# Performance work log

Measured on AMD Instinct MI355X. Metric: run time of the kernel, lower is better.

Reference implementation:

```python
import jax, jax.numpy as jnp
import numpy as np

H = 150
PASSES = 5
NSETS = 2
N = 50000
E = 400000
G = 64
SLOPE = 0.01  # torch leaky_relu default


def setup_inputs() -> dict:
    key = jax.random.key(0)
    ks = jax.random.split(key, 20)
    def u(k, shape, fan):
        lim = 1.0 / np.sqrt(fan)
        return jax.random.uniform(k, shape, jnp.float32, -lim, lim)
    return {
        "nodes": jax.random.normal(ks[0], (N, H), jnp.float32),
        "problem_type": jax.random.uniform(ks[1], (G, 1), jnp.float32),
        "edge_W": u(ks[2], (NSETS, H, H), H),
        "edge_b": u(ks[3], (NSETS, H), H),
        "gru_w_ih": u(ks[4], (3 * H, H), H),
        "gru_w_hh": u(ks[5], (3 * H, H), H),
        "gru_b_ih": u(ks[6], (3 * H,), H),
        "gru_b_hh": u(ks[7], (3 * H,), H),
        "fc1_w": u(ks[8], (80, 151), 151),
        "fc1_b": u(ks[9], (80,), 151),
        "fc2_w": u(ks[10], (80, 80), 80),
        "fc2_b": u(ks[11], (80,), 80),
        "fcL_w": u(ks[12], (10, 80), 80),
        "fcL_b": u(ks[13], (10,), 80),
        "edges": jax.random.randint(ks[14], (NSETS, E, 2), 0, N),
        "graph_ids": jnp.sort(jax.random.randint(ks[15], (N,), 0, G)),
        "tbptt": 0,
    }


def _gru_cell(x, h, w_ih, w_hh, b_ih, b_hh):
    gi = x @ w_ih.T + b_ih  # [N, 3H]
    gh = h @ w_hh.T + b_hh
    ir, iz, inn = jnp.split(gi, 3, axis=-1)
    hr, hz, hn = jnp.split(gh, 3, axis=-1)
    r = jax.nn.sigmoid(ir + hr)
    z = jax.nn.sigmoid(iz + hz)
    n = jnp.tanh(inn + r * hn)
    return (1.0 - z) * n + z * h


def reference(nodes, problem_type, edge_W, edge_b, gru_w_ih, gru_w_hh,
              gru_b_ih, gru_b_hh, fc1_w, fc1_b, fc2_w, fc2_b, fcL_w, fcL_b,
              edges, graph_ids, tbptt):
    n_sets = edge_W.shape[0]
    n_graphs = problem_type.shape[0]
    for j in range(PASSES):
        incoming = jnp.zeros_like(nodes)
        for k in range(n_sets):
            src = edges[k, :, 1]
            dst = edges[k, :, 0]
            # NOTE: in the source, the first Linear+leaky_relu result is
            # overwritten; the effective edge message is just the second Linear.
            y = nodes[src] @ edge_W[k].T + edge_b[k]  # [E, H]
            incoming = incoming.at[dst].add(y)
        nodes = _gru_cell(incoming, nodes, gru_w_ih, gru_w_hh, gru_b_ih, gru_b_hh)
        if tbptt == 1 and j < PASSES - 2:
            nodes = jax.lax.stop_gradient(nodes)
    g = jax.ops.segment_sum(nodes, graph_ids, num_segments=n_graphs)  # [G, H]
    g = jnp.log(g)
    g = jnp.where(jnp.isnan(g), 0.0, g)
    g = jax.nn.relu(g)
    x = jnp.concatenate([g, problem_type], axis=1)  # [G, 151]
    x = jax.nn.leaky_relu(x @ fc1_w.T + fc1_b, SLOPE)
    x = jax.nn.leaky_relu(x @ fc2_w.T + fc2_b, SLOPE)
    return x @ fcL_w.T + fcL_b  # [G, 10]
```

## Files before the change

### kernel.cpp

```cpp
#include <hip/hip_runtime.h>
#include <stdint.h>

#define NN 50000
#define H 150
#define NE 400000
#define NG 64
#define NPASS 5
#define KB 480
#define VC 640
#define NRB 391

typedef unsigned short u16;
typedef unsigned int u32;
typedef __attribute__((ext_vector_type(8))) short short8;
typedef __attribute__((ext_vector_type(4))) float float4v;
typedef __attribute__((ext_vector_type(4))) u32 uint4v;
typedef __attribute__((ext_vector_type(2))) u32 uint2v;

__device__ __forceinline__ u16 f2bf_rn(float x) {
  union { float f; u32 u; } v; v.f = x;
  u32 r = v.u + 0x7fffu + ((v.u >> 16) & 1u);
  return (u16)(r >> 16);
}
__device__ __forceinline__ float bf2f(u16 h) {
  union { u32 u; float f; } v; v.u = ((u32)h) << 16;
  return v.f;
}
__device__ __forceinline__ u32 packf(float v) {
  u16 hi = f2bf_rn(v);
  u16 lo = f2bf_rn(v - bf2f(hi));
  return (u32)hi | ((u32)lo << 16);
}
__device__ __forceinline__ float upk(u32 u) {
  union { u32 u; float f; } a, b;
  a.u = u << 16; b.u = u & 0xffff0000u;
  return a.f + b.f;
}
__device__ __forceinline__ void async16(const void* g, void* l) {
  __builtin_amdgcn_global_load_lds(
      (const __attribute__((address_space(1))) unsigned int*)(uintptr_t)g,
      (__attribute__((address_space(3))) unsigned int*)(uint32_t)(uintptr_t)l,
      16, 0, 0);
}

__global__ void hist_kernel(const int* __restrict__ edges, int* __restrict__ cnt) {
  int id = blockIdx.x * 256 + threadIdx.x;
  if (id >= 2 * NE) return;
  int dst = edges[id * 2];
  int set = id / NE;
  atomicAdd(&cnt[dst * 2 + set], 1);
}

__global__ __launch_bounds__(1024) void scan1_kernel(const int* __restrict__ cnt,
                                                     int* __restrict__ rowptr,
                                                     int* __restrict__ bsum, int n) {
  __shared__ int sd[1024];
  int t = threadIdx.x;
  int idx = blockIdx.x * 1024 + t;
  int v = (idx < n) ? cnt[idx] : 0;
  sd[t] = v;
  __syncthreads();
  for (int off = 1; off < 1024; off <<= 1) {
    int add = (t >= off) ? sd[t - off] : 0;
    __syncthreads();
    sd[t] += add;
    __syncthreads();
  }
  if (idx < n) rowptr[idx] = sd[t] - v;
  if (t == 1023) bsum[blockIdx.x] = sd[1023];
}

__global__ __launch_bounds__(128) void scan2_kernel(const int* __restrict__ bsum,
                                                    int* __restrict__ boff, int nb) {
  __shared__ int sd[128];
  int t = threadIdx.x;
  int v = (t < nb) ? bsum[t] : 0;
  sd[t] = v;
  __syncthreads();
  for (int off = 1; off < 128; off <<= 1) {
    int add = (t >= off) ? sd[t - off] : 0;
    __syncthreads();
    sd[t] += add;
    __syncthreads();
  }
  boff[t] = sd[t] - v;
}

__global__ void scan3_kernel(int* __restrict__ rowptr, const int* __restrict__ boff, int n) {
  int idx = blockIdx.x * 256 + threadIdx.x;
  if (idx < n) rowptr[idx] += boff[idx >> 10];
}

__global__ void total_kernel(int* __restrict__ rowptr, const int* __restrict__ boff, int n, int nb) {
  if (threadIdx.x == 0 && blockIdx.x == 0) rowptr[n] = boff[nb];
}

__global__ void copy_int_kernel(const int* __restrict__ a, int* __restrict__ b, int n) {
  int id = blockIdx.x * 256 + threadIdx.x;
  if (id < n) b[id] = a[id];
}

__global__ void fill_kernel(const int* __restrict__ edges, int* __restrict__ cursor,
                            u16* __restrict__ colbuf) {
  int id = blockIdx.x * 256 + threadIdx.x;
  if (id >= 2 * NE) return;
  int dst = edges[id * 2];
  int src = edges[id * 2 + 1];
  int set = id / NE;
  int pos = atomicAdd(&cursor[dst * 2 + set], 1);
  colbuf[pos] = (u16)src;
}

__global__ void bounds_kernel(const int* __restrict__ gids, int* __restrict__ gstart) {
  int g = threadIdx.x;
  if (g > NG) return;
  int lo = 0, hi = NN;
  while (lo < hi) { int m = (lo + hi) >> 1; if (gids[m] < g) lo = m + 1; else hi = m; }
  gstart[g] = lo;
}

__global__ void build_B_kernel(const float* __restrict__ wih, const float* __restrict__ whh,
                               const float* __restrict__ eW,
                               u16* __restrict__ Bh, u16* __restrict__ Bl) {
  int id = blockIdx.x * 256 + threadIdx.x;
  if (id >= VC * KB) return;
  int v = id / KB, k = id % KB;
  int g = (v >> 4) & 3, c = (v >> 6) * 16 + (v & 15);
  int seg = k / 160, kk = k % 160;
  float val = 0.f;
  if (c < H && kk < H) {
    if (seg < 2) {
      if (g < 3) {
        const float* wr = wih + (size_t)(g * H + c) * H;
        const float* wc = eW + (size_t)seg * H * H + kk;
        float acc = 0.f;
        for (int t = 0; t < H; t++) acc += wr[t] * wc[(size_t)t * H];
        val = acc;
      }
    } else {
      if (g == 0) val = whh[(size_t)c * H + kk];
      else if (g == 1) val = whh[(size_t)(H + c) * H + kk];
      else if (g == 3) val = whh[(size_t)(2 * H + c) * H + kk];
    }
  }
  u16 h = f2bf_rn(val);
  Bh[id] = h;
  Bl[id] = f2bf_rn(val - bf2f(h));
}

__global__ void build_coef_kernel(const float* __restrict__ wih,
                                  const float* __restrict__ eb,
                                  const float* __restrict__ bih, const float* __restrict__ bhh,
                                  float* __restrict__ coefs) {
  int id = threadIdx.x + blockIdx.x * 256;
  if (id >= VC) return;
  int g = id / 160, c = id % 160;
  float u0 = 0.f, u1 = 0.f, bs = 0.f;
  if (c < H) {
    if (g < 3) {
      const float* wr = wih + (size_t)(g * H + c) * H;
      for (int t = 0; t < H; t++) { u0 += wr[t] * eb[t]; u1 += wr[t] * eb[H + t]; }
    }
    if (g == 0) bs = bih[c] + bhh[c];
    else if (g == 1) bs = bih[H + c] + bhh[H + c];
    else if (g == 2) bs = bih[2 * H + c];
    else bs = bhh[2 * H + c];
  }
  coefs[id] = u0;
  coefs[VC + id] = u1;
  coefs[2 * VC + id] = bs;
}

__global__ void init_nodes_kernel(const float* __restrict__ nin,
                                  u32* __restrict__ npkA, u32* __restrict__ npkB) {
  int id = blockIdx.x * 256 + threadIdx.x;
  if (id >= NN * 160) return;
  int r = id / 160, c = id % 160;
  if (c < H) {
    npkA[id] = packf(nin[(size_t)r * H + c]);
  } else {
    npkA[id] = 0;
    npkB[id] = 0;
  }
}

__global__ void pad_S_kernel(u32* __restrict__ Snp) {
  int id = blockIdx.x * 256 + threadIdx.x;
  if (id >= NN * 20) return;
  int r = id / 20, rem = id % 20;
  int set = rem / 10, t = rem % 10;
  Snp[(size_t)r * 320 + set * 160 + H + t] = 0;
}

__global__ __launch_bounds__(256) void gather_kernel(
    const u32* __restrict__ npk, const int* __restrict__ rowptr,
    const u16* __restrict__ colbuf, u32* __restrict__ Snp) {
  int gtid = blockIdx.x * 256 + threadIdx.x;
  int wid = gtid >> 6;
  if (wid >= 2 * NN) return;
  int node = wid >> 1, set = wid & 1;
  int lane = gtid & 63;
  int s = rowptr[2 * node + set], e = rowptr[2 * node + set + 1];
  int deg = e - s;
  int cA = 2 * lane, cC = 128 + lane;
  bool okC = (cC < H);
  float aA = 0.f, aB = 0.f, aC = 0.f;
  for (int base = 0; base < deg; base += 64) {
    int rem = min(64, deg - base);
    u32 srcv = 0;
    if (lane < rem) srcv = (u32)colbuf[s + base + lane];
    int i = 0;
    for (; i + 3 < rem; i += 4) {
      u32 r0 = (u32)__builtin_amdgcn_readlane((int)srcv, i);
      u32 r1 = (u32)__builtin_amdgcn_readlane((int)srcv, i + 1);
      u32 r2 = (u32)__builtin_amdgcn_readlane((int)srcv, i + 2);
      u32 r3 = (u32)__builtin_amdgcn_readlane((int)srcv, i + 3);
      const u32* p0 = npk + (size_t)r0 * 160;
      const u32* p1 = npk + (size_t)r1 * 160;
      const u32* p2 = npk + (size_t)r2 * 160;
      const u32* p3 = npk + (size_t)r3 * 160;
      uint2v v0 = *(const uint2v*)(p0 + cA);
      uint2v v1 = *(const uint2v*)(p1 + cA);
      uint2v v2 = *(const uint2v*)(p2 + cA);
      uint2v v3 = *(const uint2v*)(p3 + cA);
      u32 w0 = 0, w1 = 0, w2 = 0, w3 = 0;
      if (okC) { w0 = p0[cC]; w1 = p1[cC]; w2 = p2[cC]; w3 = p3[cC]; }
      aA += upk(v0.x) + upk(v1.x);
      aB += upk(v0.y) + upk(v1.y);
      if (okC) aC += upk(w0) + upk(w1);
      aA += upk(v2.x) + upk(v3.x);
      aB += upk(v2.y) + upk(v3.y);
      if (okC) aC += upk(w2) + upk(w3);
    }
    for (; i + 1 < rem; i += 2) {
      u32 r0 = (u32)__builtin_amdgcn_readlane((int)srcv, i);
      u32 r1 = (u32)__builtin_amdgcn_readlane((int)srcv, i + 1);
      const u32* p0 = npk + (size_t)r0 * 160;
      const u32* p1 = npk + (size_t)r1 * 160;
      uint2v v0 = *(const uint2v*)(p0 + cA);
      uint2v v1 = *(const uint2v*)(p1 + cA);
      aA += upk(v0.x) + upk(v1.x);
      aB += upk(v0.y) + upk(v1.y);
      if (okC) aC += upk(p0[cC]) + upk(p1[cC]);
    }
    if (i < rem) {
      u32 r0 = (u32)__builtin_amdgcn_readlane((int)srcv, i);
      const u32* p0 = npk + (size_t)r0 * 160;
      uint2v v0 = *(const uint2v*)(p0 + cA);
      aA += upk(v0.x);
      aB += upk(v0.y);
      if (okC) aC += upk(p0[cC]);
    }
  }
  u32* o = Snp + (size_t)node * 320 + set * 160;
  o[cA] = packf(aA);
  o[cA + 1] = packf(aB);
  if (okC) o[cC] = packf(aC);
}


template<int KT>
__device__ __forceinline__ void stage_fn(
    const u32* __restrict__ Snp, const u32* __restrict__ npkc,
    const u16* __restrict__ Bhp, const u16* __restrict__ Blp,
    char* Ab, char* Bb, int tid, int w, int r0, int ccb) {
  #pragma unroll
  for (int i = 0; i < 4; i++) {
    int cl = i * 256 + tid;
    int row = cl >> 3;
    int q = (cl & 7) ^ (row & 7);
    int rg = min(r0 + row, NN - 1);
    if constexpr (KT < 10)
      async16(Snp + (size_t)rg * 320 + KT * 32 + q * 4, Ab + i * 4096 + w * 1024);
    else
      async16(npkc + (size_t)rg * 160 + (KT - 10) * 32 + q * 4, Ab + i * 4096 + w * 1024);
  }
  constexpr int koffB = (KT < 10) ? KT * 32 : 320 + (KT - 10) * 32;
  constexpr int skipg = (KT < 10) ? 3 : 2;
  #pragma unroll
  for (int i = 0; i < 2; i++) {
    int cl = i * 256 + tid;
    int row = cl >> 2;
    int q = (cl & 3) ^ ((row >> 1) & 3);
    if (((row >> 4) & 3) != skipg) {
      size_t gb = (size_t)(ccb * 128 + row) * KB + koffB + q * 8;
      int lb = i * 4096 + w * 1024;
      async16(Bhp + gb, Bb + lb);
      async16(Blp + gb, Bb + 8192 + lb);
    }
  }
}

template<int KTn>
__device__ __forceinline__ void read_frags_fn(
    const char* Ab, const char* Bb, int m, int quad, int mrow0, int nco0,
    uint4v (&A0)[4], uint4v (&A1)[4], short8 (&RBh)[3], short8 (&RBl)[3]) {
  #pragma unroll
  for (int jj = 0; jj < 3; jj++) {
    const int jsel = (jj == 2) ? ((KTn < 10) ? 2 : 3) : jj;
    int br = nco0 + jsel * 16 + m;
    int bd = br * 64 + ((quad ^ ((br >> 1) & 3)) * 16);
    RBh[jj] = *(const short8*)(Bb + bd);
    RBl[jj] = *(const short8*)(Bb + 8192 + bd);
  }
  #pragma unroll
  for (int mt = 0; mt < 4; mt++) {
    int r = mrow0 + mt * 16 + m;
    A0[mt] = *(const uint4v*)(Ab + r * 128 + (((2 * quad) ^ (r & 7)) * 16));
    A1[mt] = *(const uint4v*)(Ab + r * 128 + (((2 * quad + 1) ^ (r & 7)) * 16));
  }
}

template<int KT>
__device__ __forceinline__ void mfma_fn(
    const uint4v (&A0)[4], const uint4v (&A1)[4],
    const short8 (&MBh)[3], const short8 (&MBl)[3], float4v (&acc)[4][4]) {
  #pragma unroll
  for (int mt = 0; mt < 4; mt++) {
    u32 uu[8] = {A0[mt].x, A0[mt].y, A0[mt].z, A0[mt].w,
                 A1[mt].x, A1[mt].y, A1[mt].z, A1[mt].w};
    short8 ah, al;
    #pragma unroll
    for (int e2 = 0; e2 < 8; e2++) {
      ah[e2] = (short)(uu[e2] & 0xffffu);
      al[e2] = (short)(uu[e2] >> 16);
    }
    #pragma unroll
    for (int jj = 0; jj < 3; jj++) {
      const int J = (KT < 10) ? jj : ((jj == 2) ? 3 : jj);
      acc[mt][J] = __builtin_amdgcn_mfma_f32_16x16x32_bf16(ah, MBh[jj], acc[mt][J], 0, 0, 0);
      acc[mt][J] = __builtin_amdgcn_mfma_f32_16x16x32_bf16(ah, MBl[jj], acc[mt][J], 0, 0, 0);
      acc[mt][J] = __builtin_amdgcn_mfma_f32_16x16x32_bf16(al, MBh[jj], acc[mt][J], 0, 0, 0);
    }
  }
}

template<int KT>
__device__ __forceinline__ void gemm_step(
    const u32* __restrict__ Snp, const u32* __restrict__ npkc,
    const u16* __restrict__ Bhp, const u16* __restrict__ Blp,
    char (&Abuf)[16384], char (&Bbuf)[16384],
    int tid, int w, int m, int quad, int mrow0, int nco0, int r0, int ccb,
    float4v (&acc)[4][4]) {
  uint4v A0[4], A1[4];
  short8 FBh[3], FBl[3];
  read_frags_fn<KT>(Abuf, Bbuf, m, quad, mrow0, nco0, A0, A1, FBh, FBl);
  asm volatile("s_waitcnt lgkmcnt(0)" ::: "memory");
  __builtin_amdgcn_sched_barrier(0);
  __builtin_amdgcn_s_barrier();
  if constexpr (KT + 1 <= 14)
    stage_fn<KT + 1>(Snp, npkc, Bhp, Blp, Abuf, Bbuf, tid, w, r0, ccb);
  __builtin_amdgcn_sched_barrier(0);
  __builtin_amdgcn_s_setprio(1);
  mfma_fn<KT>(A0, A1, FBh, FBl, acc);
  __builtin_amdgcn_s_setprio(0);
  __builtin_amdgcn_sched_barrier(0);
  if constexpr (KT + 1 <= 14) {
    asm volatile("s_waitcnt vmcnt(0)" ::: "memory");
    __builtin_amdgcn_sched_barrier(0);
    __builtin_amdgcn_s_barrier();
  }
}

__global__ __launch_bounds__(256, 4) void gru_gemm_kernel(
    const u32* __restrict__ Snp, const u32* __restrict__ npkc,
    const u16* __restrict__ Bhp, const u16* __restrict__ Blp,
    const float* __restrict__ coefs, const int* __restrict__ rowptr,
    u32* __restrict__ npkn) {
  __shared__ char Abuf[16384];
  __shared__ char Bbuf[16384];
  const int bid = blockIdx.x;
  const int xcd = bid & 7;
  const int rest = bid >> 3;
  const int ccb = rest % 5;
  const int r0b = (rest / 5) * 8 + xcd;
  if (r0b >= NRB) return;
  const int r0 = r0b * 128;
  const int tid = threadIdx.x;
  const int w = tid >> 6, l = tid & 63;
  const int m = l & 15, quad = l >> 4;
  const int mrow0 = (w & 1) * 64;
  const int nco0 = (w >> 1) * 64;

  float4v acc[4][4];
  #pragma unroll
  for (int mt = 0; mt < 4; mt++)
    #pragma unroll
    for (int j = 0; j < 4; j++) acc[mt][j] = (float4v){0.f, 0.f, 0.f, 0.f};

  stage_fn<0>(Snp, npkc, Bhp, Blp, Abuf, Bbuf, tid, w, r0, ccb);
  asm volatile("s_waitcnt vmcnt(0)" ::: "memory");
  __builtin_amdgcn_sched_barrier(0);
  __builtin_amdgcn_s_barrier();

  #define STEP(K) gemm_step<K>(Snp, npkc, Bhp, Blp, Abuf, Bbuf, tid, w, m, quad, \
                               mrow0, nco0, r0, ccb, acc)
  STEP(0);  STEP(1);  STEP(2);  STEP(3);  STEP(4);
  STEP(5);  STEP(6);  STEP(7);  STEP(8);  STEP(9);
  STEP(10); STEP(11); STEP(12); STEP(13); STEP(14);
  #undef STEP

  int c = (ccb * 2 + (w >> 1)) * 16 + m;
  if (c >= H) return;
  float u0r = coefs[c],            u0z = coefs[160 + c],
        u0n = coefs[320 + c];
  float u1r = coefs[VC + c],       u1z = coefs[VC + 160 + c],
        u1n = coefs[VC + 320 + c];
  float bsr = coefs[2 * VC + c],   bsz = coefs[2 * VC + 160 + c],
        bsn = coefs[2 * VC + 320 + c], bsh = coefs[2 * VC + 480 + c];
  #pragma unroll
  for (int mt = 0; mt < 4; mt++) {
    #pragma unroll
    for (int i = 0; i < 4; i++) {
      int row = r0 + mrow0 + mt * 16 + quad * 4 + i;
      if (row >= NN) continue;
      float d0 = (float)(rowptr[2 * row + 1] - rowptr[2 * row]);
      float d1 = (float)(rowptr[2 * row + 2] - rowptr[2 * row + 1]);
      float pr = acc[mt][0][i] + d0 * u0r + d1 * u1r + bsr;
      float pz = acc[mt][1][i] + d0 * u0z + d1 * u1z + bsz;
      float pn = acc[mt][2][i] + d0 * u0n + d1 * u1n + bsn;
      float ph = acc[mt][3][i] + bsh;
      float r_g = 1.f / (1.f + __expf(-pr));
      float z_g = 1.f / (1.f + __expf(-pz));
      float narg = pn + r_g * ph;
      float e2 = __expf(2.f * narg);
      float n_g = 1.f - 2.f / (e2 + 1.f);
      float h = upk(npkc[(size_t)row * 160 + c]);
      npkn[(size_t)row * 160 + c] = packf((1.f - z_g) * n_g + z_g * h);
    }
  }
}

__global__ __launch_bounds__(192) void segsum_kernel(const u32* __restrict__ npk,
                                                     const int* __restrict__ gstart,
                                                     float* __restrict__ gsum) {
  int g = blockIdx.x, chunk = blockIdx.y;
  int c = threadIdx.x;
  if (c >= H) return;
  int s = gstart[g], e = gstart[g + 1];
  int len = e - s;
  if (len <= 0) return;
  int per = (len + 3) / 4;
  int rs = s + chunk * per;
  int re = min(e, rs + per);
  if (rs >= re) return;
  float acc = 0.f;
  for (int r = rs; r < re; r++) acc += upk(npk[(size_t)r * 160 + c]);
  atomicAdd(&gsum[g * H + c], acc);
}

__global__ __launch_bounds__(192) void head_kernel(
    const float* __restrict__ gsum, const float* __restrict__ pt,
    const float* __restrict__ fc1_w, const float* __restrict__ fc1_b,
    const float* __restrict__ fc2_w, const float* __restrict__ fc2_b,
    const float* __restrict__ fcL_w, const float* __restrict__ fcL_b,
    float* __restrict__ out) {
  __shared__ float x[151];
  __shared__ float x1[80];
  __shared__ float x2[80];
  int row = blockIdx.x;
  int t = threadIdx.x;
  if (t < 151) {
    float v;
    if (t < H) { float g = gsum[row * H + t]; v = (g > 1.f) ? logf(g) : 0.f; }
    else v = pt[row];
    x[t] = v;
  }
  __syncthreads();
  if (t < 80) {
    float acc = fc1_b[t];
    const float* wrow = fc1_w + t * 151;
    #pragma unroll 4
    for (int k = 0; k < 151; k++) acc += x[k] * wrow[k];
    x1[t] = (acc > 0.f) ? acc : 0.01f * acc;
  }
  __syncthreads();
  if (t < 80) {
    float acc = fc2_b[t];
    const float* wrow = fc2_w + t * 80;
    #pragma unroll 4
    for (int k = 0; k < 80; k++) acc += x1[k] * wrow[k];
    x2[t] = (acc > 0.f) ? acc : 0.01f * acc;
  }
  __syncthreads();
  if (t < 10) {
    float acc = fcL_b[t];
    const float* wrow = fcL_w + t * 80;
    #pragma unroll 4
    for (int k = 0; k < 80; k++) acc += x2[k] * wrow[k];
    out[row * 10 + t] = acc;
  }
}

extern "C" void kernel_launch(void* const* d_in, const int* in_sizes, int n_in,
                              void* d_out, int out_size, void* d_ws, size_t ws_size,
                              hipStream_t stream) {
  const float* nodes_in = (const float*)d_in[0];
  const float* problem_type = (const float*)d_in[1];
  const float* edge_W = (const float*)d_in[2];
  const float* edge_b = (const float*)d_in[3];
  const float* w_ih = (const float*)d_in[4];
  const float* w_hh = (const float*)d_in[5];
  const float* b_ih = (const float*)d_in[6];
  const float* b_hh = (const float*)d_in[7];
  const float* fc1_w = (const float*)d_in[8];
  const float* fc1_b = (const float*)d_in[9];
  const float* fc2_w = (const float*)d_in[10];
  const float* fc2_b = (const float*)d_in[11];
  const float* fcL_w = (const float*)d_in[12];
  const float* fcL_b = (const float*)d_in[13];
  const int* edges = (const int*)d_in[14];
  const int* graph_ids = (const int*)d_in[15];

  char* ws = (char*)d_ws;
  size_t off = 0;
  auto alloc = [&](size_t bytes) -> void* {
    void* p = ws + off;
    off = (off + bytes + 255) & ~(size_t)255;
    return p;
  };
  u32* npkA     = (u32*)alloc((size_t)NN * 160 * 4);
  u32* npkB     = (u32*)alloc((size_t)NN * 160 * 4);
  u32* Snp      = (u32*)alloc((size_t)NN * 320 * 4);
  u16* Bh       = (u16*)alloc((size_t)VC * KB * 2);
  u16* Bl       = (u16*)alloc((size_t)VC * KB * 2);
  float* coefs  = (float*)alloc(3 * VC * 4);
  int* rowptr   = (int*)alloc((2 * NN + 1) * 4);
  int* cursor   = (int*)alloc(2 * NN * 4);
  u16* colbuf   = (u16*)alloc(2ull * NE * 2);
  int* bsum     = (int*)alloc(128 * 4);
  int* boff     = (int*)alloc(128 * 4);
  int* gstart   = (int*)alloc((NG + 1) * 4);
  float* gsum   = (float*)alloc((size_t)NG * H * 4);

  const int n2 = 2 * NN;
  const int nb = (n2 + 1023) / 1024;

  hipMemsetAsync(cursor, 0, n2 * 4, stream);
  hist_kernel<<<(2 * NE + 255) / 256, 256, 0, stream>>>(edges, cursor);
  scan1_kernel<<<nb, 1024, 0, stream>>>(cursor, rowptr, bsum, n2);
  scan2_kernel<<<1, 128, 0, stream>>>(bsum, boff, nb);
  scan3_kernel<<<(n2 + 255) / 256, 256, 0, stream>>>(rowptr, boff, n2);
  total_kernel<<<1, 64, 0, stream>>>(rowptr, boff, n2, nb);
  copy_int_kernel<<<(n2 + 255) / 256, 256, 0, stream>>>(rowptr, cursor, n2);
  fill_kernel<<<(2 * NE + 255) / 256, 256, 0, stream>>>(edges, cursor, colbuf);
  bounds_kernel<<<1, 128, 0, stream>>>(graph_ids, gstart);
  build_B_kernel<<<(VC * KB + 255) / 256, 256, 0, stream>>>(w_ih, w_hh, edge_W, Bh, Bl);
  build_coef_kernel<<<(VC + 255) / 256, 256, 0, stream>>>(w_ih, edge_b, b_ih, b_hh, coefs);
  init_nodes_kernel<<<(NN * 160 + 255) / 256, 256, 0, stream>>>(nodes_in, npkA, npkB);
  pad_S_kernel<<<(NN * 20 + 255) / 256, 256, 0, stream>>>(Snp);

  const int ngrp = (NRB + 7) / 8;
  u32* nbuf[2] = {npkA, npkB};
  for (int pass = 0; pass < NPASS; pass++) {
    u32* cur = nbuf[pass & 1];
    u32* nxt = nbuf[1 - (pass & 1)];
    gather_kernel<<<(2 * NN * 64 + 255) / 256, 256, 0, stream>>>(cur, rowptr, colbuf, Snp);
    gru_gemm_kernel<<<ngrp * 5 * 8, 256, 0, stream>>>(
        Snp, cur, Bh, Bl, coefs, rowptr, nxt);
  }
  u32* fin = nbuf[NPASS & 1];

  hipMemsetAsync(gsum, 0, (size_t)NG * H * 4, stream);
  segsum_kernel<<<dim3(NG, 4), 192, 0, stream>>>(fin, gstart, gsum);
  head_kernel<<<NG, 192, 0, stream>>>(gsum, problem_type, fc1_w, fc1_b, fc2_w, fc2_b,
                                      fcL_w, fcL_b, (float*)d_out);
}
```

Before: 1.129 ms.

## Split packed hi/lo bf16 node and message buffers into separate planar arrays

```diff
diff --git a/kernel.cpp b/kernel.cpp
--- a/kernel.cpp
+++ b/kernel.cpp
@@ -14,8 +14,6 @@
 typedef unsigned int u32;
 typedef __attribute__((ext_vector_type(8))) short short8;
 typedef __attribute__((ext_vector_type(4))) float float4v;
-typedef __attribute__((ext_vector_type(4))) u32 uint4v;
-typedef __attribute__((ext_vector_type(2))) u32 uint2v;
 
 __device__ __forceinline__ u16 f2bf_rn(float x) {
   union { float f; u32 u; } v; v.f = x;
@@ -30,11 +28,6 @@
   u16 hi = f2bf_rn(v);
   u16 lo = f2bf_rn(v - bf2f(hi));
   return (u32)hi | ((u32)lo << 16);
-}
-__device__ __forceinline__ float upk(u32 u) {
-  union { u32 u; float f; } a, b;
-  a.u = u << 16; b.u = u & 0xffff0000u;
-  return a.f + b.f;
 }
 __device__ __forceinline__ void async16(const void* g, void* l) {
   __builtin_amdgcn_global_load_lds(
@@ -172,29 +165,31 @@
 }
 
 __global__ void init_nodes_kernel(const float* __restrict__ nin,
-                                  u32* __restrict__ npkA, u32* __restrict__ npkB) {
+                                  u16* __restrict__ nhA, u16* __restrict__ nlA,
+                                  u16* __restrict__ nhB, u16* __restrict__ nlB) {
   int id = blockIdx.x * 256 + threadIdx.x;
   if (id >= NN * 160) return;
   int r = id / 160, c = id % 160;
-  if (c < H) {
-    npkA[id] = packf(nin[(size_t)r * H + c]);
-  } else {
-    npkA[id] = 0;
-    npkB[id] = 0;
-  }
-}
-
-__global__ void pad_S_kernel(u32* __restrict__ Snp) {
+  u32 pw = 0;
+  if (c < H) pw = packf(nin[(size_t)r * H + c]);
+  nhA[id] = (u16)pw;
+  nlA[id] = (u16)(pw >> 16);
+  if (c >= H) { nhB[id] = 0; nlB[id] = 0; }
+}
+
+__global__ void pad_S_kernel(u16* __restrict__ Sh, u16* __restrict__ Sl) {
   int id = blockIdx.x * 256 + threadIdx.x;
   if (id >= NN * 20) return;
   int r = id / 20, rem = id % 20;
   int set = rem / 10, t = rem % 10;
-  Snp[(size_t)r * 320 + set * 160 + H + t] = 0;
+  size_t off = (size_t)r * 320 + set * 160 + H + t;
+  Sh[off] = 0; Sl[off] = 0;
 }
 
 __global__ __launch_bounds__(256) void gather_kernel(
-    const u32* __restrict__ npk, const int* __restrict__ rowptr,
-    const u16* __restrict__ colbuf, u32* __restrict__ Snp) {
+    const u16* __restrict__ nh, const u16* __restrict__ nl,
+    const int* __restrict__ rowptr, const u16* __restrict__ colbuf,
+    u16* __restrict__ Sh, u16* __restrict__ Sl) {
   int gtid = blockIdx.x * 256 + threadIdx.x;
   int wid = gtid >> 6;
   if (wid >= 2 * NN) return;
@@ -202,79 +197,95 @@
   int lane = gtid & 63;
   int s = rowptr[2 * node + set], e = rowptr[2 * node + set + 1];
   int deg = e - s;
-  int cA = 2 * lane, cC = 128 + lane;
-  bool okC = (cC < H);
-  float aA = 0.f, aB = 0.f, aC = 0.f;
+  int cA = 2 * lane, cC = 128 + 2 * lane;
+  bool okC = (lane < 11);
+  float aA = 0.f, aB = 0.f, aC = 0.f, aD = 0.f;
   for (int base = 0; base < deg; base += 64) {
     int rem = min(64, deg - base);
     u32 srcv = 0;
     if (lane < rem) srcv = (u32)colbuf[s + base + lane];
     int i = 0;
     for (; i + 3 < rem; i += 4) {
-      u32 r0 = (u32)__builtin_amdgcn_readlane((int)srcv, i);
-      u32 r1 = (u32)__builtin_amdgcn_readlane((int)srcv, i + 1);
-      u32 r2 = (u32)__builtin_amdgcn_readlane((int)srcv, i + 2);
-      u32 r3 = (u32)__builtin_amdgcn_readlane((int)srcv, i + 3);
-      const u32* p0 = npk + (size_t)r0 * 160;
-      const u32* p1 = npk + (size_t)r1 * 160;
-      const u32* p2 = npk + (size_t)r2 * 160;
-      const u32* p3 = npk + (size_t)r3 * 160;
-      uint2v v0 = *(const uint2v*)(p0 + cA);
-      uint2v v1 = *(const uint2v*)(p1 + cA);
-      uint2v v2 = *(const uint2v*)(p2 + cA);
-      uint2v v3 = *(const uint2v*)(p3 + cA);
-      u32 w0 = 0, w1 = 0, w2 = 0, w3 = 0;
-      if (okC) { w0 = p0[cC]; w1 = p1[cC]; w2 = p2[cC]; w3 = p3[cC]; }
-      aA += upk(v0.x) + upk(v1.x);
-      aB += upk(v0.y) + upk(v1.y);
-      if (okC) aC += upk(w0) + upk(w1);
-      aA += upk(v2.x) + upk(v3.x);
-      aB += upk(v2.y) + upk(v3.y);
-      if (okC) aC += upk(w2) + upk(w3);
+      int r0 = __builtin_amdgcn_readlane((int)srcv, i);
+      int r1 = __builtin_amdgcn_readlane((int)srcv, i + 1);
+      int r2 = __builtin_amdgcn_readlane((int)srcv, i + 2);
+      int r3 = __builtin_amdgcn_readlane((int)srcv, i + 3);
+      const u16* h0 = nh + (size_t)(u32)r0 * 160; const u16* L0 = nl + (size_t)(u32)r0 * 160;
+      const u16* h1 = nh + (size_t)(u32)r1 * 160; const u16* L1 = nl + (size_t)(u32)r1 * 160;
+      const u16* h2 = nh + (size_t)(u32)r2 * 160; const u16* L2 = nl + (size_t)(u32)r2 * 160;
+      const u16* h3 = nh + (size_t)(u32)r3 * 160; const u16* L3 = nl + (size_t)(u32)r3 * 160;
+      u32 vh0 = *(const u32*)(h0 + cA), vl0 = *(const u32*)(L0 + cA);
+      u32 vh1 = *(const u32*)(h1 + cA), vl1 = *(const u32*)(L1 + cA);
+      u32 vh2 = *(const u32*)(h2 + cA), vl2 = *(const u32*)(L2 + cA);
+      u32 vh3 = *(const u32*)(h3 + cA), vl3 = *(const u32*)(L3 + cA);
+      u32 wh0 = 0, wl0 = 0, wh1 = 0, wl1 = 0, wh2 = 0, wl2 = 0, wh3 = 0, wl3 = 0;
+      if (okC) {
+        wh0 = *(const u32*)(h0 + cC); wl0 = *(const u32*)(L0 + cC);
+        wh1 = *(const u32*)(h1 + cC); wl1 = *(const u32*)(L1 + cC);
+        wh2 = *(const u32*)(h2 + cC); wl2 = *(const u32*)(L2 + cC);
+        wh3 = *(const u32*)(h3 + cC); wl3 = *(const u32*)(L3 + cC);
+      }
+      aA += (bf2f((u16)vh0) + bf2f((u16)vl0)) + (bf2f((u16)vh1) + bf2f((u16)vl1));
+      aB += (bf2f((u16)(vh0 >> 16)) + bf2f((u16)(vl0 >> 16))) + (bf2f((u16)(vh1 >> 16)) + bf2f((u16)(vl1 >> 16)));
+      if (okC) {
+        aC += (bf2f((u16)wh0) + bf2f((u16)wl0)) + (bf2f((u16)wh1) + bf2f((u16)wl1));
+        aD += (bf2f((u16)(wh0 >> 16)) + bf2f((u16)(wl0 >> 16))) + (bf2f((u16)(wh1 >> 16)) + bf2f((u16)(wl1 >> 16)));
+      }
+      aA += (bf2f((u16)vh2) + bf2f((u16)vl2)) + (bf2f((u16)vh3) + bf2f((u16)vl3));
+      aB += (bf2f((u16)(vh2 >> 16)) + bf2f((u16)(vl2 >> 16))) + (bf2f((u16)(vh3 >> 16)) + bf2f((u16)(vl3 >> 16)));
+      if (okC) {
+        aC += (bf2f((u16)wh2) + bf2f((u16)wl2)) + (bf2f((u16)wh3) + bf2f((u16)wl3));
+        aD += (bf2f((u16)(wh2 >> 16)) + bf2f((u16)(wl2 >> 16))) + (bf2f((u16)(wh3 >> 16)) + bf2f((u16)(wl3 >> 16)));
+      }
     }
     for (; i + 1 < rem; i += 2) {
-      u32 r0 = (u32)__builtin_amdgcn_readlane((int)srcv, i);
-      u32 r1 = (u32)__builtin_amdgcn_readlane((int)srcv, i + 1);
-      const u32* p0 = npk + (size_t)r0 * 160;
-      const u32* p1 = npk + (size_t)r1 * 160;
-      uint2v v0 = *(const uint2v*)(p0 + cA);
-      uint2v v1 = *(const uint2v*)(p1 + cA);
-      aA += upk(v0.x) + upk(v1.x);
-      aB += upk(v0.y) + upk(v1.y);
-      if (okC) aC += upk(p0[cC]) + upk(p1[cC]);
+      int r0 = __builtin_amdgcn_readlane((int)srcv, i);
+      int r1 = __builtin_amdgcn_readlane((int)srcv, i + 1);
+      const u16* h0 = nh + (size_t)(u32)r0 * 160; const u16* L0 = nl + (size_t)(u32)r0 * 160;
+      const u16* h1 = nh + (size_t)(u32)r1 * 160; const u16* L1 = nl + (size_t)(u32)r1 * 160;
+      u32 vh0 = *(const u32*)(h0 + cA), vl0 = *(const u32*)(L0 + cA);
+      u32 vh1 = *(const u32*)(h1 + cA), vl1 = *(const u32*)(L1 + cA);
+      aA += (bf2f((u16)vh0) + bf2f((u16)vl0)) + (bf2f((u16)vh1) + bf2f((u16)vl1));
+      aB += (bf2f((u16)(vh0 >> 16)) + bf2f((u16)(vl0 >> 16))) + (bf2f((u16)(vh1 >> 16)) + bf2f((u16)(vl1 >> 16)));
+      if (okC) {
+        u32 wh0 = *(const u32*)(h0 + cC), wl0 = *(const u32*)(L0 + cC);
+        u32 wh1 = *(const u32*)(h1 + cC), wl1 = *(const u32*)(L1 + cC);
+        aC += (bf2f((u16)wh0) + bf2f((u16)wl0)) + (bf2f((u16)wh1) + bf2f((u16)wl1));
+        aD += (bf2f((u16)(wh0 >> 16)) + bf2f((u16)(wl0 >> 16))) + (bf2f((u16)(wh1 >> 16)) + bf2f((u16)(wl1 >> 16)));
+      }
     }
     if (i < rem) {
-      u32 r0 = (u32)__builtin_amdgcn_readlane((int)srcv, i);
-      const u32* p0 = npk + (size_t)r0 * 160;
-      uint2v v0 = *(const uint2v*)(p0 + cA);
-      aA += upk(v0.x);
-      aB += upk(v0.y);
-      if (okC) aC += upk(p0[cC]);
-    }
-  }
-  u32* o = Snp + (size_t)node * 320 + set * 160;
-  o[cA] = packf(aA);
-  o[cA + 1] = packf(aB);
-  if (okC) o[cC] = packf(aC);
+      int r0 = __builtin_amdgcn_readlane((int)srcv, i);
+      const u16* h0 = nh + (size_t)(u32)r0 * 160; const u16* L0 = nl + (size_t)(u32)r0 * 160;
+      u32 vh0 = *(const u32*)(h0 + cA), vl0 = *(const u32*)(L0 + cA);
+      aA += bf2f((u16)vh0) + bf2f((u16)vl0);
+      aB += bf2f((u16)(vh0 >> 16)) + bf2f((u16)(vl0 >> 16));
+      if (okC) {
+        u32 wh0 = *(const u32*)(h0 + cC), wl0 = *(const u32*)(L0 + cC);
+        aC += bf2f((u16)wh0) + bf2f((u16)wl0);
+        aD += bf2f((u16)(wh0 >> 16)) + bf2f((u16)(wl0 >> 16));
+      }
+    }
+  }
+  u16* oh = Sh + (size_t)node * 320 + set * 160;
+  u16* ol = Sl + (size_t)node * 320 + set * 160;
+  u32 pA = packf(aA), pB = packf(aB);
+  *(u32*)(oh + cA) = (pA & 0xffffu) | (pB << 16);
+  *(u32*)(ol + cA) = (pA >> 16) | (pB & 0xffff0000u);
+  if (okC) {
+    u32 pC = packf(aC), pD = packf(aD);
+    *(u32*)(oh + cC) = (pC & 0xffffu) | (pD << 16);
+    *(u32*)(ol + cC) = (pC >> 16) | (pD & 0xffff0000u);
+  }
 }
 
 
 template<int KT>
 __device__ __forceinline__ void stage_fn(
-    const u32* __restrict__ Snp, const u32* __restrict__ npkc,
+    const u16* __restrict__ Shp, const u16* __restrict__ Slp,
+    const u16* __restrict__ nhc, const u16* __restrict__ nlc,
     const u16* __restrict__ Bhp, const u16* __restrict__ Blp,
     char* Ab, char* Bb, int tid, int w, int r0, int ccb) {
-  #pragma unroll
-  for (int i = 0; i < 4; i++) {
-    int cl = i * 256 + tid;
-    int row = cl >> 3;
-    int q = (cl & 7) ^ (row & 7);
-    int rg = min(r0 + row, NN - 1);
-    if constexpr (KT < 10)
-      async16(Snp + (size_t)rg * 320 + KT * 32 + q * 4, Ab + i * 4096 + w * 1024);
-    else
-      async16(npkc + (size_t)rg * 160 + (KT - 10) * 32 + q * 4, Ab + i * 4096 + w * 1024);
-  }
   constexpr int koffB = (KT < 10) ? KT * 32 : 320 + (KT - 10) * 32;
   constexpr int skipg = (KT < 10) ? 3 : 2;
   #pragma unroll
@@ -282,9 +293,19 @@
     int cl = i * 256 + tid;
     int row = cl >> 2;
     int q = (cl & 3) ^ ((row >> 1) & 3);
+    int rg = min(r0 + row, NN - 1);
+    int lb = i * 4096 + w * 1024;
+    if constexpr (KT < 10) {
+      size_t go = (size_t)rg * 320 + KT * 32 + q * 8;
+      async16(Shp + go, Ab + lb);
+      async16(Slp + go, Ab + 8192 + lb);
+    } else {
+      size_t go = (size_t)rg * 160 + (KT - 10) * 32 + q * 8;
+      async16(nhc + go, Ab + lb);
+      async16(nlc + go, Ab + 8192 + lb);
+    }
     if (((row >> 4) & 3) != skipg) {
       size_t gb = (size_t)(ccb * 128 + row) * KB + koffB + q * 8;
-      int lb = i * 4096 + w * 1024;
       async16(Bhp + gb, Bb + lb);
       async16(Blp + gb, Bb + 8192 + lb);
     }
@@ -294,7 +315,7 @@
 template<int KTn>
 __device__ __forceinline__ void read_frags_fn(
     const char* Ab, const char* Bb, int m, int quad, int mrow0, int nco0,
-    uint4v (&A0)[4], uint4v (&A1)[4], short8 (&RBh)[3], short8 (&RBl)[3]) {
+    short8 (&Ah)[4], short8 (&Al)[4], short8 (&RBh)[3], short8 (&RBl)[3]) {
   #pragma unroll
   for (int jj = 0; jj < 3; jj++) {
     const int jsel = (jj == 2) ? ((KTn < 10) ? 2 : 3) : jj;
@@ -306,53 +327,46 @@
   #pragma unroll
   for (int mt = 0; mt < 4; mt++) {
     int r = mrow0 + mt * 16 + m;
-    A0[mt] = *(const uint4v*)(Ab + r * 128 + (((2 * quad) ^ (r & 7)) * 16));
-    A1[mt] = *(const uint4v*)(Ab + r * 128 + (((2 * quad + 1) ^ (r & 7)) * 16));
+    int ad = r * 64 + ((quad ^ ((r >> 1) & 3)) * 16);
+    Ah[mt] = *(const short8*)(Ab + ad);
+    Al[mt] = *(const short8*)(Ab + 8192 + ad);
   }
 }
 
 template<int KT>
 __device__ __forceinline__ void mfma_fn(
-    const uint4v (&A0)[4], const uint4v (&A1)[4],
+    const short8 (&Ah)[4], const short8 (&Al)[4],
     const short8 (&MBh)[3], const short8 (&MBl)[3], float4v (&acc)[4][4]) {
   #pragma unroll
   for (int mt = 0; mt < 4; mt++) {
-    u32 uu[8] = {A0[mt].x, A0[mt].y, A0[mt].z, A0[mt].w,
-                 A1[mt].x, A1[mt].y, A1[mt].z, A1[mt].w};
-    short8 ah, al;
-    #pragma unroll
-    for (int e2 = 0; e2 < 8; e2++) {
-      ah[e2] = (short)(uu[e2] & 0xffffu);
-      al[e2] = (short)(uu[e2] >> 16);
-    }
     #pragma unroll
     for (int jj = 0; jj < 3; jj++) {
       const int J = (KT < 10) ? jj : ((jj == 2) ? 3 : jj);
-      acc[mt][J] = __builtin_amdgcn_mfma_f32_16x16x32_bf16(ah, MBh[jj], acc[mt][J], 0, 0, 0);
-      acc[mt][J] = __builtin_amdgcn_mfma_f32_16x16x32_bf16(ah, MBl[jj], acc[mt][J], 0, 0, 0);
-      acc[mt][J] = __builtin_amdgcn_mfma_f32_16x16x32_bf16(al, MBh[jj], acc[mt][J], 0, 0, 0);
+      acc[mt][J] = __builtin_amdgcn_mfma_f32_16x16x32_bf16(Ah[mt], MBh[jj], acc[mt][J], 0, 0, 0);
+      acc[mt][J] = __builtin_amdgcn_mfma_f32_16x16x32_bf16(Ah[mt], MBl[jj], acc[mt][J], 0, 0, 0);
+      acc[mt][J] = __builtin_amdgcn_mfma_f32_16x16x32_bf16(Al[mt], MBh[jj], acc[mt][J], 0, 0, 0);
     }
   }
 }
 
 template<int KT>
 __device__ __forceinline__ void gemm_step(
-    const u32* __restrict__ Snp, const u32* __restrict__ npkc,
+    const u16* __restrict__ Shp, const u16* __restrict__ Slp,
+    const u16* __restrict__ nhc, const u16* __restrict__ nlc,
     const u16* __restrict__ Bhp, const u16* __restrict__ Blp,
     char (&Abuf)[16384], char (&Bbuf)[16384],
     int tid, int w, int m, int quad, int mrow0, int nco0, int r0, int ccb,
     float4v (&acc)[4][4]) {
-  uint4v A0[4], A1[4];
-  short8 FBh[3], FBl[3];
-  read_frags_fn<KT>(Abuf, Bbuf, m, quad, mrow0, nco0, A0, A1, FBh, FBl);
+  short8 Ah[4], Al[4], FBh[3], FBl[3];
+  read_frags_fn<KT>(Abuf, Bbuf, m, quad, mrow0, nco0, Ah, Al, FBh, FBl);
   asm volatile("s_waitcnt lgkmcnt(0)" ::: "memory");
   __builtin_amdgcn_sched_barrier(0);
   __builtin_amdgcn_s_barrier();
   if constexpr (KT + 1 <= 14)
-    stage_fn<KT + 1>(Snp, npkc, Bhp, Blp, Abuf, Bbuf, tid, w, r0, ccb);
+    stage_fn<KT + 1>(Shp, Slp, nhc, nlc, Bhp, Blp, Abuf, Bbuf, tid, w, r0, ccb);
   __builtin_amdgcn_sched_barrier(0);
   __builtin_amdgcn_s_setprio(1);
-  mfma_fn<KT>(A0, A1, FBh, FBl, acc);
+  mfma_fn<KT>(Ah, Al, FBh, FBl, acc);
   __builtin_amdgcn_s_setprio(0);
   __builtin_amdgcn_sched_barrier(0);
   if constexpr (KT + 1 <= 14) {
@@ -363,10 +377,11 @@
 }
 
 __global__ __launch_bounds__(256, 4) void gru_gemm_kernel(
-    const u32* __restrict__ Snp, const u32* __restrict__ npkc,
+    const u16* __restrict__ Shp, const u16* __restrict__ Slp,
+    const u16* __restrict__ nhc, const u16* __restrict__ nlc,
     const u16* __restrict__ Bhp, const u16* __restrict__ Blp,
     const float* __restrict__ coefs, const int* __restrict__ rowptr,
-    u32* __restrict__ npkn) {
+    u16* __restrict__ nhn, u16* __restrict__ nln) {
   __shared__ char Abuf[16384];
   __shared__ char Bbuf[16384];
   const int bid = blockIdx.x;
@@ -388,13 +403,13 @@
     #pragma unroll
     for (int j = 0; j < 4; j++) acc[mt][j] = (float4v){0.f, 0.f, 0.f, 0.f};
 
-  stage_fn<0>(Snp, npkc, Bhp, Blp, Abuf, Bbuf, tid, w, r0, ccb);
+  stage_fn<0>(Shp, Slp, nhc, nlc, Bhp, Blp, Abuf, Bbuf, tid, w, r0, ccb);
   asm volatile("s_waitcnt vmcnt(0)" ::: "memory");
   __builtin_amdgcn_sched_barrier(0);
   __builtin_amdgcn_s_barrier();
 
-  #define STEP(K) gemm_step<K>(Snp, npkc, Bhp, Blp, Abuf, Bbuf, tid, w, m, quad, \
-                               mrow0, nco0, r0, ccb, acc)
+  #define STEP(K) gemm_step<K>(Shp, Slp, nhc, nlc, Bhp, Blp, Abuf, Bbuf, tid, w, \
+                               m, quad, mrow0, nco0, r0, ccb, acc)
   STEP(0);  STEP(1);  STEP(2);  STEP(3);  STEP(4);
   STEP(5);  STEP(6);  STEP(7);  STEP(8);  STEP(9);
   STEP(10); STEP(11); STEP(12); STEP(13); STEP(14);
@@ -425,13 +440,17 @@
       float narg = pn + r_g * ph;
       float e2 = __expf(2.f * narg);
       float n_g = 1.f - 2.f / (e2 + 1.f);
-      float h = upk(npkc[(size_t)row * 160 + c]);
-      npkn[(size_t)row * 160 + c] = packf((1.f - z_g) * n_g + z_g * h);
-    }
-  }
-}
-
-__global__ __launch_bounds__(192) void segsum_kernel(const u32* __restrict__ npk,
+      size_t off = (size_t)row * 160 + c;
+      float h = bf2f(nhc[off]) + bf2f(nlc[off]);
+      u32 pw = packf((1.f - z_g) * n_g + z_g * h);
+      nhn[off] = (u16)pw;
+      nln[off] = (u16)(pw >> 16);
+    }
+  }
+}
+
+__global__ __launch_bounds__(192) void segsum_kernel(const u16* __restrict__ nh,
+                                                     const u16* __restrict__ nl,
                                                      const int* __restrict__ gstart,
                                                      float* __restrict__ gsum) {
   int g = blockIdx.x, chunk = blockIdx.y;
@@ -445,7 +464,10 @@
   int re = min(e, rs + per);
   if (rs >= re) return;
   float acc = 0.f;
-  for (int r = rs; r < re; r++) acc += upk(npk[(size_t)r * 160 + c]);
+  for (int r = rs; r < re; r++) {
+    size_t off = (size_t)r * 160 + c;
+    acc += bf2f(nh[off]) + bf2f(nl[off]);
+  }
   atomicAdd(&gsum[g * H + c], acc);
 }
 
@@ -519,9 +541,12 @@
     off = (off + bytes + 255) & ~(size_t)255;
     return p;
   };
-  u32* npkA     = (u32*)alloc((size_t)NN * 160 * 4);
-  u32* npkB     = (u32*)alloc((size_t)NN * 160 * 4);
-  u32* Snp      = (u32*)alloc((size_t)NN * 320 * 4);
+  u16* nhA      = (u16*)alloc((size_t)NN * 160 * 2);
+  u16* nlA      = (u16*)alloc((size_t)NN * 160 * 2);
+  u16* nhB      = (u16*)alloc((size_t)NN * 160 * 2);
+  u16* nlB      = (u16*)alloc((size_t)NN * 160 * 2);
+  u16* Sh       = (u16*)alloc((size_t)NN * 320 * 2);
+  u16* Sl       = (u16*)alloc((size_t)NN * 320 * 2);
   u16* Bh       = (u16*)alloc((size_t)VC * KB * 2);
   u16* Bl       = (u16*)alloc((size_t)VC * KB * 2);
   float* coefs  = (float*)alloc(3 * VC * 4);
@@ -547,22 +572,27 @@
   bounds_kernel<<<1, 128, 0, stream>>>(graph_ids, gstart);
   build_B_kernel<<<(VC * KB + 255) / 256, 256, 0, stream>>>(w_ih, w_hh, edge_W, Bh, Bl);
   build_coef_kernel<<<(VC + 255) / 256, 256, 0, stream>>>(w_ih, edge_b, b_ih, b_hh, coefs);
-  init_nodes_kernel<<<(NN * 160 + 255) / 256, 256, 0, stream>>>(nodes_in, npkA, npkB);
-  pad_S_kernel<<<(NN * 20 + 255) / 256, 256, 0, stream>>>(Snp);
+  init_nodes_kernel<<<(NN * 160 + 255) / 256, 256, 0, stream>>>(nodes_in, nhA, nlA, nhB, nlB);
+  pad_S_kernel<<<(NN * 20 + 255) / 256, 256, 0, stream>>>(Sh, Sl);
 
   const int ngrp = (NRB + 7) / 8;
-  u32* nbuf[2] = {npkA, npkB};
+  u16* nhb[2] = {nhA, nhB};
+  u16* nlb[2] = {nlA, nlB};
   for (int pass = 0; pass < NPASS; pass++) {
-    u32* cur = nbuf[pass & 1];
-    u32* nxt = nbuf[1 - (pass & 1)];
-    gather_kernel<<<(2 * NN * 64 + 255) / 256, 256, 0, stream>>>(cur, rowptr, colbuf, Snp);
+    u16* nhc = nhb[pass & 1];
+    u16* nlc = nlb[pass & 1];
+    u16* nhn = nhb[1 - (pass & 1)];
+    u16* nln = nlb[1 - (pass & 1)];
+    gather_kernel<<<(2 * NN * 64 + 255) / 256, 256, 0, stream>>>(
+        nhc, nlc, rowptr, colbuf, Sh, Sl);
     gru_gemm_kernel<<<ngrp * 5 * 8, 256, 0, stream>>>(
-        Snp, cur, Bh, Bl, coefs, rowptr, nxt);
-  }
-  u32* fin = nbuf[NPASS & 1];
+        Sh, Sl, nhc, nlc, Bh, Bl, coefs, rowptr, nhn, nln);
+  }
+  u16* finh = nhb[NPASS & 1];
+  u16* finl = nlb[NPASS & 1];
 
   hipMemsetAsync(gsum, 0, (size_t)NG * H * 4, stream);
-  segsum_kernel<<<dim3(NG, 4), 192, 0, stream>>>(fin, gstart, gsum);
+  segsum_kernel<<<dim3(NG, 4), 192, 0, stream>>>(finh, finl, gstart, gsum);
   head_kernel<<<NG, 192, 0, stream>>>(gsum, problem_type, fc1_w, fc1_b, fc2_w, fc2_b,
                                       fcL_w, fcL_b, (float*)d_out);
 }
```

Result: slower. 1.254 ms (+11.1%).
